# Kernel tuning notes

Hardware: AMD Instinct MI355X
Metric: run time of the kernel (lower is better)

## Reference

```python
import jax, jax.numpy as jnp
import numpy as np

B, N, H, HEADS = 4, 2048, 1024, 16
D = H // HEADS  # head dim = 64

def rotate_half(x):
    x1, x2 = jnp.split(x, 2, axis=-1)
    return jnp.concatenate((-x2, x1), axis=-1)

def apply_rope(pos, t):
    # pos: [n, d] broadcasts against t: [b, h, n, d]
    return t * jnp.cos(pos) + rotate_half(t) * jnp.sin(pos)

def setup_inputs() -> dict:
    key = jax.random.key(0)
    k1, k2, k3, k4 = jax.random.split(key, 4)
    x = jax.random.normal(k1, (B, N, H), dtype=jnp.float32)
    rotary_emb = jax.random.normal(k2, (N, D), dtype=jnp.float32)
    # torch Linear(H, 3H, bias=False): weight [3H, H], y = x @ W.T
    w_qkv = jax.random.normal(k3, (3 * H, H), dtype=jnp.float32) * (1.0 / np.sqrt(H))
    w_out = jax.random.normal(k4, (H, H), dtype=jnp.float32) * (1.0 / np.sqrt(H))
    return {"x": x, "rotary_emb": rotary_emb, "w_qkv": w_qkv, "w_out": w_out}

def reference(x, rotary_emb, w_qkv, w_out):
    qkv = jnp.einsum('bnh,oh->bno', x, w_qkv)  # [B, N, 3H]
    q, k, v = jnp.split(qkv, 3, axis=-1)
    def split_heads(t):
        return t.reshape(B, N, HEADS, D).transpose(0, 2, 1, 3)  # b h n d
    q, k, v = map(split_heads, (q, k, v))
    q = apply_rope(rotary_emb, q)
    k = apply_rope(rotary_emb, k)
    scale = 1.0 / np.sqrt(D).astype(np.float32)
    scores = jnp.einsum('bhqd,bhkd->bhqk', q, k) * scale
    attn = jax.nn.softmax(scores, axis=-1)
    out = jnp.einsum('bhqk,bhkd->bhqd', attn, v)
    out = out.transpose(0, 2, 1, 3).reshape(B, N, H)  # b n (h d)
    return jnp.einsum('bnh,oh->bno', out, w_out)
```

## Files before the change

### kernel.cpp

```cpp
#include <hip/hip_runtime.h>
#include <hip/hip_fp16.h>
#include <stdint.h>

#define DEVI __device__ __forceinline__

using f16x2 = __attribute__((ext_vector_type(2))) _Float16;
using f16x8 = __attribute__((ext_vector_type(8))) _Float16;
using f32x4 = __attribute__((ext_vector_type(4))) float;
using f32x16 = __attribute__((ext_vector_type(16))) float;
using u32x4 = __attribute__((ext_vector_type(4))) uint32_t;

DEVI void gload_lds16(const void* g, void* lds) {
  using GP = const __attribute__((address_space(1))) void*;
  using LP = __attribute__((address_space(3))) void*;
  __builtin_amdgcn_global_load_lds((GP)g, (LP)lds, 16, 0, 0);
}

DEVI uint32_t pack2h(float a, float b) {
  return (uint32_t)__half_as_ushort(__float2half(a)) |
         ((uint32_t)__half_as_ushort(__float2half(b)) << 16);
}

DEVI uint32_t cvtpk(float a, float b) {
  auto h2 = __builtin_amdgcn_cvt_pkrtz(a, b);
  return __builtin_bit_cast(uint32_t, h2);
}

DEVI void plswap(uint32_t& a, uint32_t& b) {
  asm volatile("v_permlane32_swap_b32 %0, %1" : "+v"(a), "+v"(b));
}

DEVI float dot2acc(uint32_t w, f16x2 one, float c) {
  return __builtin_amdgcn_fdot2(__builtin_bit_cast(f16x2, w), one, c, false);
}

DEVI float fmax3(float a, float b, float c) { return fmaxf(fmaxf(a, b), c); }

__global__ __launch_bounds__(256) void cvt_f32_f16(const float* __restrict__ in,
                                                   __half* __restrict__ out, int n8) {
  int i = blockIdx.x * 256 + threadIdx.x;
  if (i >= n8) return;
  float4 a = ((const float4*)in)[i * 2];
  float4 b = ((const float4*)in)[i * 2 + 1];
  uint4 u;
  u.x = pack2h(a.x, a.y);
  u.y = pack2h(a.z, a.w);
  u.z = pack2h(b.x, b.y);
  u.w = pack2h(b.z, b.w);
  ((uint4*)out)[i] = u;
}

DEVI void store_c(__half* p, float v) { *p = __float2half(v); }
DEVI void store_c(float* p, float v) { *p = v; }

template <typename OT>
__global__ __launch_bounds__(256) void gemm_bt(const __half* __restrict__ A,
                                               const __half* __restrict__ B,
                                               OT* __restrict__ C, int M, int N, int K) {
  __shared__ __half As[128 * 32];
  __shared__ __half Bs[128 * 32];
  const int tid = threadIdx.x;
  const int w = tid >> 6, l = tid & 63;
  const int wm = w >> 1, wn = w & 1;
  const int m16 = l & 15, g = l >> 4;
  const int row0 = blockIdx.y * 128, col0 = blockIdx.x * 128;

  const int srow = l >> 2;
  const int ks = ((l & 3) ^ (srow & 3)) * 8;

  f32x4 acc[4][4] = {};

  for (int kt = 0; kt < K; kt += 32) {
    __syncthreads();
#pragma unroll
    for (int i = 0; i < 2; ++i) {
      int c = w * 2 + i;
      int r = c * 16 + srow;
      gload_lds16(A + (size_t)(row0 + r) * K + kt + ks, (char*)As + c * 1024);
      gload_lds16(B + (size_t)(col0 + r) * K + kt + ks, (char*)Bs + c * 1024);
    }
    __syncthreads();
    f16x8 aF[4], bF[4];
#pragma unroll
    for (int mi = 0; mi < 4; ++mi) {
      int r = wm * 64 + mi * 16 + m16;
      aF[mi] = *(const f16x8*)((const char*)As + r * 64 + ((g << 4) ^ ((r & 3) << 4)));
    }
#pragma unroll
    for (int ni = 0; ni < 4; ++ni) {
      int r = wn * 64 + ni * 16 + m16;
      bF[ni] = *(const f16x8*)((const char*)Bs + r * 64 + ((g << 4) ^ ((r & 3) << 4)));
    }
#pragma unroll
    for (int mi = 0; mi < 4; ++mi)
#pragma unroll
      for (int ni = 0; ni < 4; ++ni)
        acc[mi][ni] = __builtin_amdgcn_mfma_f32_16x16x32_f16(aF[mi], bF[ni], acc[mi][ni], 0, 0, 0);
  }

#pragma unroll
  for (int mi = 0; mi < 4; ++mi)
#pragma unroll
    for (int ni = 0; ni < 4; ++ni)
#pragma unroll
      for (int j = 0; j < 4; ++j) {
        int r = row0 + wm * 64 + mi * 16 + g * 4 + j;
        int cc = col0 + wn * 64 + ni * 16 + m16;
        store_c(&C[(size_t)r * N + cc], acc[mi][ni][j]);
      }
}

__global__ __launch_bounds__(256) void rope_scatter(const __half* __restrict__ qkv,
                                                    const float* __restrict__ rot,
                                                    __half* __restrict__ qr,
                                                    __half* __restrict__ kr,
                                                    __half* __restrict__ vr) {
  int t = blockIdx.x * 256 + threadIdx.x;
  int s = t >> 17;
  int rem = t & 131071;
  int bh = rem >> 11;
  int n = rem & 2047;
  int b = bh >> 4, h = bh & 15;
  const __half* src = qkv + (size_t)(b * 2048 + n) * 3072 + s * 1024 + h * 64;
  if (s == 2) {
    __half* vdst = vr + ((size_t)bh * 64) * 2048 + n;
#pragma unroll
    for (int c = 0; c < 8; ++c) {
      f16x8 vv = ((const f16x8*)src)[c];
#pragma unroll
      for (int j = 0; j < 8; ++j) vdst[(size_t)(c * 8 + j) * 2048] = vv[j];
    }
    return;
  }
  __half* dst = (s == 0 ? qr : kr) + ((size_t)bh * 2048 + n) * 64;
  const float sc = (s == 0) ? 0.18033688011112042f : 1.0f;
  const float* rp = rot + n * 64;
#pragma unroll
  for (int c = 0; c < 4; ++c) {
    f16x8 lo = ((const f16x8*)src)[c];
    f16x8 hi = ((const f16x8*)src)[c + 4];
    float ol[8], oh[8];
#pragma unroll
    for (int j = 0; j < 8; ++j) {
      int d = c * 8 + j;
      float tl = (float)lo[j], th = (float)hi[j];
      float s0, c0, s1, c1;
      __sincosf(rp[d], &s0, &c0);
      __sincosf(rp[d + 32], &s1, &c1);
      ol[j] = (tl * c0 - th * s0) * sc;
      oh[j] = (th * c1 + tl * s1) * sc;
    }
    uint4 ulo, uhi;
    ulo.x = pack2h(ol[0], ol[1]); ulo.y = pack2h(ol[2], ol[3]);
    ulo.z = pack2h(ol[4], ol[5]); ulo.w = pack2h(ol[6], ol[7]);
    uhi.x = pack2h(oh[0], oh[1]); uhi.y = pack2h(oh[2], oh[3]);
    uhi.z = pack2h(oh[4], oh[5]); uhi.w = pack2h(oh[6], oh[7]);
    ((uint4*)dst)[c] = ulo;
    ((uint4*)dst)[c + 4] = uhi;
  }
}

__global__ __launch_bounds__(256, 4) void attn_fwd(const __half* __restrict__ qr,
                                                   const __half* __restrict__ kr,
                                                   const __half* __restrict__ vr,
                                                   __half* __restrict__ out) {
  __shared__ __half K2[2 * 64 * 64];
  __shared__ __half V2[2 * 64 * 64];

  int bid = blockIdx.x;
  bid = (bid & 7) * 128 + (bid >> 3);
  const int bh = bid >> 4;
  const int q0 = (bid & 15) * 128;
  const int tid = threadIdx.x;
  const int w = tid >> 6, l = tid & 63;
  const int q = l & 31, hi = l >> 5;
  const size_t headoff = (size_t)bh * 2048 * 64;

  f16x8 qB[4];
  {
    const __half* qp = qr + headoff + (size_t)(q0 + w * 32 + q) * 64 + hi * 8;
#pragma unroll
    for (int c = 0; c < 4; ++c) qB[c] = *(const f16x8*)(qp + c * 16);
  }

  int kf[4];
#pragma unroll
  for (int c = 0; c < 4; ++c)
    kf[c] = q * 128 + 16 * (hi ^ (q & 1)) + 32 * (c ^ ((q >> 1) & 3));
  const int vbase = q * 128 + ((hi ^ (q & 7)) << 4);

  const int krow_l = l >> 3, kslot = l & 7;
  const __half* kb = kr + headoff;
  const __half* vb = vr + (size_t)bh * 64 * 2048;

  auto STAGE = [&](int buf, int kv0) {
#pragma unroll
    for (int i = 0; i < 2; ++i) {
      int c = w * 2 + i;
      int row = c * 8 + krow_l;
      gload_lds16(kb + (size_t)(kv0 + row) * 64 + ((kslot ^ (row & 7)) * 8),
                  (char*)K2 + buf * 8192 + c * 1024);
    }
#pragma unroll
    for (int i = 0; i < 2; ++i) {
      int c = w * 2 + i;
      int d = c * 8 + (l >> 3);
      gload_lds16(vb + (size_t)d * 2048 + kv0 + (((l & 7) ^ (l >> 3)) * 8),
                  (char*)V2 + buf * 8192 + c * 1024);
    }
  };

  const f16x2 one2 = {(_Float16)1.f, (_Float16)1.f};
  f32x16 o0 = {}, o1 = {};
  float mreg = -1e30f, lreg = 0.f;

  STAGE(0, 0);
  __syncthreads();

  for (int t = 0; t < 32; ++t) {
    const int buf = t & 1;
    if (t < 31) STAGE(buf ^ 1, (t + 1) * 64);

    const char* Kb = (const char*)K2 + buf * 8192;
    const char* Vb = (const char*)V2 + buf * 8192;
#pragma unroll
    for (int kvb = 0; kvb < 2; ++kvb) {
      f32x16 s = {};
      __builtin_amdgcn_s_setprio(1);
#pragma unroll
      for (int c = 0; c < 4; ++c) {
        f16x8 kA = *(const f16x8*)(Kb + kvb * 4096 + kf[c]);
        s = __builtin_amdgcn_mfma_f32_32x32x16_f16(kA, qB[c], s, 0, 0, 0);
      }
      __builtin_amdgcn_s_setprio(0);

      float mt = fmax3(s[0], s[1], s[2]);
      mt = fmax3(mt, s[3], s[4]);
      mt = fmax3(mt, s[5], s[6]);
      mt = fmax3(mt, s[7], s[8]);
      mt = fmax3(mt, s[9], s[10]);
      mt = fmax3(mt, s[11], s[12]);
      mt = fmax3(mt, s[13], s[14]);
      mt = fmaxf(mt, s[15]);
      mt = fmaxf(mt, __shfl_xor(mt, 32));
      if (__any(mt - mreg > 8.f)) {
        float mnew = fmaxf(mreg, mt);
        float alpha = __builtin_amdgcn_exp2f(mreg - mnew);
        lreg *= alpha;
        o0 *= alpha;
        o1 *= alpha;
        mreg = mnew;
      }
      uint32_t W[8];
      float rs = 0.f;
#pragma unroll
      for (int i2 = 0; i2 < 8; ++i2) {
        float e0 = __builtin_amdgcn_exp2f(s[2 * i2] - mreg);
        float e1 = __builtin_amdgcn_exp2f(s[2 * i2 + 1] - mreg);
        W[i2] = cvtpk(e0, e1);
        rs = dot2acc(W[i2], one2, rs);
      }
      rs += __shfl_xor(rs, 32);
      lreg += rs;

      plswap(W[0], W[2]);
      plswap(W[1], W[3]);
      plswap(W[4], W[6]);
      plswap(W[5], W[7]);
      u32x4 f0 = {W[0], W[1], W[2], W[3]};
      u32x4 f1 = {W[4], W[5], W[6], W[7]};
      f16x8 pA0 = __builtin_bit_cast(f16x8, f0);
      f16x8 pA1 = __builtin_bit_cast(f16x8, f1);

      const int vx = vbase ^ (kvb << 6);
      const int vx2 = vx ^ 32;
      f16x8 v00 = *(const f16x8*)(Vb + vx);
      f16x8 v01 = *(const f16x8*)(Vb + vx + 4096);
      f16x8 v10 = *(const f16x8*)(Vb + vx2);
      f16x8 v11 = *(const f16x8*)(Vb + vx2 + 4096);
      __builtin_amdgcn_s_setprio(1);
      o0 = __builtin_amdgcn_mfma_f32_32x32x16_f16(pA0, v00, o0, 0, 0, 0);
      o1 = __builtin_amdgcn_mfma_f32_32x32x16_f16(pA0, v01, o1, 0, 0, 0);
      o0 = __builtin_amdgcn_mfma_f32_32x32x16_f16(pA1, v10, o0, 0, 0, 0);
      o1 = __builtin_amdgcn_mfma_f32_32x32x16_f16(pA1, v11, o1, 0, 0, 0);
      __builtin_amdgcn_s_setprio(0);
    }

    __syncthreads();
  }

  const int b = bh >> 4, hh = bh & 15;
  float invl = 1.0f / lreg;
#pragma unroll
  for (int r = 0; r < 16; ++r) {
    int qrow = (r & 3) + 8 * (r >> 2) + 4 * hi;
    float inv = __shfl(invl, qrow);
    __half* orow = out + (size_t)(b * 2048 + q0 + w * 32 + qrow) * 1024 + hh * 64;
    orow[q] = __float2half(o0[r] * inv);
    orow[32 + q] = __float2half(o1[r] * inv);
  }
}

extern "C" void kernel_launch(void* const* d_in, const int* in_sizes, int n_in,
                              void* d_out, int out_size, void* d_ws, size_t ws_size,
                              hipStream_t stream) {
  const float* x    = (const float*)d_in[0];
  const float* rot  = (const float*)d_in[1];
  const float* wqkv = (const float*)d_in[2];
  const float* wout = (const float*)d_in[3];
  float* out = (float*)d_out;
  char* ws = (char*)d_ws;

  __half* xb    = (__half*)(ws + 0);
  __half* wqkvb = (__half*)(ws + (16ull << 20));
  __half* woutb = (__half*)(ws + (22ull << 20));
  __half* qkv   = (__half*)(ws + (24ull << 20));
  __half* kr    = (__half*)(ws + (72ull << 20));
  __half* vr    = (__half*)(ws + (88ull << 20));
  __half* qr    = xb;
  __half* ao    = qkv;

  cvt_f32_f16<<<4096, 256, 0, stream>>>(x, xb, 1048576);
  cvt_f32_f16<<<1536, 256, 0, stream>>>(wqkv, wqkvb, 393216);
  cvt_f32_f16<<<512, 256, 0, stream>>>(wout, woutb, 131072);
  gemm_bt<__half><<<dim3(24, 64), 256, 0, stream>>>(xb, wqkvb, qkv, 8192, 3072, 1024);
  rope_scatter<<<1536, 256, 0, stream>>>(qkv, rot, qr, kr, vr);
  attn_fwd<<<1024, 256, 0, stream>>>(qr, kr, vr, ao);
  gemm_bt<float><<<dim3(8, 64), 256, 0, stream>>>(ao, woutb, out, 8192, 1024, 1024);
}
```

Baseline: 262.9 us.

## Fuse RoPE and head scatter into QKV GEMM epilogue, widen GEMM K-tile to 64

Removes the separate rope_scatter kernel by applying rotary embedding, the softmax scale and the head-major/transposed-V scatter directly from GEMM accumulators. This drops the fp16 qkv intermediate write and its re-read. Both GEMMs also now stage 64-wide K tiles with an 8-way XOR swizzle, halving the loop trips and barriers. Risks: the epilogue stores are scalar halfs, and the V transpose writes are strided and uncoalesced.

```diff
diff --git a/kernel.cpp b/kernel.cpp
--- a/kernel.cpp
+++ b/kernel.cpp
@@ -50,54 +50,98 @@
   ((uint4*)out)[i] = u;
 }
 
-DEVI void store_c(__half* p, float v) { *p = __float2half(v); }
-DEVI void store_c(float* p, float v) { *p = v; }
-
-template <typename OT>
-__global__ __launch_bounds__(256) void gemm_bt(const __half* __restrict__ A,
-                                               const __half* __restrict__ B,
-                                               OT* __restrict__ C, int M, int N, int K) {
-  __shared__ __half As[128 * 32];
-  __shared__ __half Bs[128 * 32];
-  const int tid = threadIdx.x;
-  const int w = tid >> 6, l = tid & 63;
-  const int wm = w >> 1, wn = w & 1;
-  const int m16 = l & 15, g = l >> 4;
-  const int row0 = blockIdx.y * 128, col0 = blockIdx.x * 128;
-
-  const int srow = l >> 2;
-  const int ks = ((l & 3) ^ (srow & 3)) * 8;
-
-  f32x4 acc[4][4] = {};
-
-  for (int kt = 0; kt < K; kt += 32) {
-    __syncthreads();
-#pragma unroll
-    for (int i = 0; i < 2; ++i) {
-      int c = w * 2 + i;
-      int r = c * 16 + srow;
-      gload_lds16(A + (size_t)(row0 + r) * K + kt + ks, (char*)As + c * 1024);
-      gload_lds16(B + (size_t)(col0 + r) * K + kt + ks, (char*)Bs + c * 1024);
-    }
-    __syncthreads();
-    f16x8 aF[4], bF[4];
-#pragma unroll
-    for (int mi = 0; mi < 4; ++mi) {
-      int r = wm * 64 + mi * 16 + m16;
-      aF[mi] = *(const f16x8*)((const char*)As + r * 64 + ((g << 4) ^ ((r & 3) << 4)));
-    }
-#pragma unroll
-    for (int ni = 0; ni < 4; ++ni) {
-      int r = wn * 64 + ni * 16 + m16;
-      bF[ni] = *(const f16x8*)((const char*)Bs + r * 64 + ((g << 4) ^ ((r & 3) << 4)));
-    }
+#define GEMM_CORE(A_, B_, K_)                                                           \
+  __shared__ __half As[128 * 64];                                                       \
+  __shared__ __half Bs[128 * 64];                                                       \
+  const int tid = threadIdx.x;                                                          \
+  const int w = tid >> 6, l = tid & 63;                                                 \
+  const int wm = w >> 1, wn = w & 1;                                                    \
+  const int m16 = l & 15, g = l >> 4;                                                   \
+  const int row0 = blockIdx.y * 128, col0 = blockIdx.x * 128;                           \
+  const int srow = l >> 3;                                                              \
+  const int ks = ((l & 7) ^ srow) * 8;                                                  \
+  f32x4 acc[4][4] = {};                                                                 \
+  for (int kt = 0; kt < (K_); kt += 64) {                                               \
+    __syncthreads();                                                                    \
+    _Pragma("unroll") for (int i = 0; i < 4; ++i) {                                     \
+      int c = w * 4 + i;                                                                \
+      int r = c * 8 + srow;                                                             \
+      gload_lds16((A_) + (size_t)(row0 + r) * (K_) + kt + ks, (char*)As + c * 1024);    \
+      gload_lds16((B_) + (size_t)(col0 + r) * (K_) + kt + ks, (char*)Bs + c * 1024);    \
+    }                                                                                   \
+    __syncthreads();                                                                    \
+    _Pragma("unroll") for (int kk = 0; kk < 2; ++kk) {                                  \
+      f16x8 aF[4], bF[4];                                                               \
+      _Pragma("unroll") for (int mi = 0; mi < 4; ++mi) {                                \
+        int r = wm * 64 + mi * 16 + m16;                                                \
+        aF[mi] = *(const f16x8*)((const char*)As + r * 128 + (((kk * 4 + g) ^ (r & 7)) << 4)); \
+      }                                                                                 \
+      _Pragma("unroll") for (int ni = 0; ni < 4; ++ni) {                                \
+        int r = wn * 64 + ni * 16 + m16;                                                \
+        bF[ni] = *(const f16x8*)((const char*)Bs + r * 128 + (((kk * 4 + g) ^ (r & 7)) << 4)); \
+      }                                                                                 \
+      _Pragma("unroll") for (int mi = 0; mi < 4; ++mi)                                  \
+          _Pragma("unroll") for (int ni = 0; ni < 4; ++ni)                              \
+              acc[mi][ni] = __builtin_amdgcn_mfma_f32_16x16x32_f16(aF[mi], bF[ni],      \
+                                                                   acc[mi][ni], 0, 0, 0); \
+    }                                                                                   \
+  }
+
+__global__ __launch_bounds__(256) void gemm_qkv_rope(const __half* __restrict__ A,
+                                                     const __half* __restrict__ B,
+                                                     const float* __restrict__ rot,
+                                                     __half* __restrict__ qr,
+                                                     __half* __restrict__ kr,
+                                                     __half* __restrict__ vr) {
+  GEMM_CORE(A, B, 1024)
+
+  const int s = blockIdx.x >> 3;
+  const int hh = (blockIdx.x & 7) * 2 + wn;
+  if (s < 2) {
+    const float sc = (s == 0) ? 0.18033688011112042f : 1.0f;
+    __half* base = (s == 0) ? qr : kr;
 #pragma unroll
     for (int mi = 0; mi < 4; ++mi)
 #pragma unroll
-      for (int ni = 0; ni < 4; ++ni)
-        acc[mi][ni] = __builtin_amdgcn_mfma_f32_16x16x32_f16(aF[mi], bF[ni], acc[mi][ni], 0, 0, 0);
-  }
-
+      for (int j = 0; j < 4; ++j) {
+        int r = row0 + wm * 64 + mi * 16 + g * 4 + j;
+        int n = r & 2047;
+        int bh = (r >> 11) * 16 + hh;
+        __half* orow = base + ((size_t)bh * 2048 + n) * 64;
+        const float* rp = rot + n * 64;
+#pragma unroll
+        for (int ni = 0; ni < 2; ++ni) {
+          int dlo = ni * 16 + m16;
+          float xlo = acc[mi][ni][j], xhi = acc[mi][ni + 2][j];
+          float s0, c0, s1, c1;
+          __sincosf(rp[dlo], &s0, &c0);
+          __sincosf(rp[dlo + 32], &s1, &c1);
+          orow[dlo]      = __float2half((xlo * c0 - xhi * s0) * sc);
+          orow[dlo + 32] = __float2half((xhi * c1 + xlo * s1) * sc);
+        }
+      }
+  } else {
+#pragma unroll
+    for (int mi = 0; mi < 4; ++mi)
+#pragma unroll
+      for (int j = 0; j < 4; ++j) {
+        int r = row0 + wm * 64 + mi * 16 + g * 4 + j;
+        int n = r & 2047;
+        int bh = (r >> 11) * 16 + hh;
+        __half* vcol = vr + ((size_t)bh * 64) * 2048 + n;
+#pragma unroll
+        for (int ni = 0; ni < 4; ++ni) {
+          int d = ni * 16 + m16;
+          vcol[(size_t)d * 2048] = __float2half(acc[mi][ni][j]);
+        }
+      }
+  }
+}
+
+__global__ __launch_bounds__(256) void gemm_bt_f32(const __half* __restrict__ A,
+                                                   const __half* __restrict__ B,
+                                                   float* __restrict__ C, int N, int K) {
+  GEMM_CORE(A, B, K)
 #pragma unroll
   for (int mi = 0; mi < 4; ++mi)
 #pragma unroll
@@ -106,58 +150,8 @@
       for (int j = 0; j < 4; ++j) {
         int r = row0 + wm * 64 + mi * 16 + g * 4 + j;
         int cc = col0 + wn * 64 + ni * 16 + m16;
-        store_c(&C[(size_t)r * N + cc], acc[mi][ni][j]);
-      }
-}
-
-__global__ __launch_bounds__(256) void rope_scatter(const __half* __restrict__ qkv,
-                                                    const float* __restrict__ rot,
-                                                    __half* __restrict__ qr,
-                                                    __half* __restrict__ kr,
-                                                    __half* __restrict__ vr) {
-  int t = blockIdx.x * 256 + threadIdx.x;
-  int s = t >> 17;
-  int rem = t & 131071;
-  int bh = rem >> 11;
-  int n = rem & 2047;
-  int b = bh >> 4, h = bh & 15;
-  const __half* src = qkv + (size_t)(b * 2048 + n) * 3072 + s * 1024 + h * 64;
-  if (s == 2) {
-    __half* vdst = vr + ((size_t)bh * 64) * 2048 + n;
-#pragma unroll
-    for (int c = 0; c < 8; ++c) {
-      f16x8 vv = ((const f16x8*)src)[c];
-#pragma unroll
-      for (int j = 0; j < 8; ++j) vdst[(size_t)(c * 8 + j) * 2048] = vv[j];
-    }
-    return;
-  }
-  __half* dst = (s == 0 ? qr : kr) + ((size_t)bh * 2048 + n) * 64;
-  const float sc = (s == 0) ? 0.18033688011112042f : 1.0f;
-  const float* rp = rot + n * 64;
-#pragma unroll
-  for (int c = 0; c < 4; ++c) {
-    f16x8 lo = ((const f16x8*)src)[c];
-    f16x8 hi = ((const f16x8*)src)[c + 4];
-    float ol[8], oh[8];
-#pragma unroll
-    for (int j = 0; j < 8; ++j) {
-      int d = c * 8 + j;
-      float tl = (float)lo[j], th = (float)hi[j];
-      float s0, c0, s1, c1;
-      __sincosf(rp[d], &s0, &c0);
-      __sincosf(rp[d + 32], &s1, &c1);
-      ol[j] = (tl * c0 - th * s0) * sc;
-      oh[j] = (th * c1 + tl * s1) * sc;
-    }
-    uint4 ulo, uhi;
-    ulo.x = pack2h(ol[0], ol[1]); ulo.y = pack2h(ol[2], ol[3]);
-    ulo.z = pack2h(ol[4], ol[5]); ulo.w = pack2h(ol[6], ol[7]);
-    uhi.x = pack2h(oh[0], oh[1]); uhi.y = pack2h(oh[2], oh[3]);
-    uhi.z = pack2h(oh[4], oh[5]); uhi.w = pack2h(oh[6], oh[7]);
-    ((uint4*)dst)[c] = ulo;
-    ((uint4*)dst)[c + 4] = uhi;
-  }
+        C[(size_t)r * N + cc] = acc[mi][ni][j];
+      }
 }
 
 __global__ __launch_bounds__(256, 4) void attn_fwd(const __half* __restrict__ qr,
@@ -314,17 +308,15 @@
   __half* xb    = (__half*)(ws + 0);
   __half* wqkvb = (__half*)(ws + (16ull << 20));
   __half* woutb = (__half*)(ws + (22ull << 20));
-  __half* qkv   = (__half*)(ws + (24ull << 20));
+  __half* qr    = (__half*)(ws + (24ull << 20));
+  __half* ao    = (__half*)(ws + (40ull << 20));
   __half* kr    = (__half*)(ws + (72ull << 20));
   __half* vr    = (__half*)(ws + (88ull << 20));
-  __half* qr    = xb;
-  __half* ao    = qkv;
 
   cvt_f32_f16<<<4096, 256, 0, stream>>>(x, xb, 1048576);
   cvt_f32_f16<<<1536, 256, 0, stream>>>(wqkv, wqkvb, 393216);
   cvt_f32_f16<<<512, 256, 0, stream>>>(wout, woutb, 131072);
-  gemm_bt<__half><<<dim3(24, 64), 256, 0, stream>>>(xb, wqkvb, qkv, 8192, 3072, 1024);
-  rope_scatter<<<1536, 256, 0, stream>>>(qkv, rot, qr, kr, vr);
+  gemm_qkv_rope<<<dim3(24, 64), 256, 0, stream>>>(xb, wqkvb, rot, qr, kr, vr);
   attn_fwd<<<1024, 256, 0, stream>>>(qr, kr, vr, ao);
-  gemm_bt<float><<<dim3(8, 64), 256, 0, stream>>>(ao, woutb, out, 8192, 1024, 1024);
-}
+  gemm_bt_f32<<<dim3(8, 64), 256, 0, stream>>>(ao, woutb, out, 1024, 1024);
+}
```

New measurement: 217.6 us. 1.21x faster.
